# Performance work log

Hardware: AMD Instinct MI355X
Metric: run time of the kernel (lower is better)

## Reference

```python
import jax, jax.numpy as jnp
import numpy as np

N_NODES = 50000
N_EDGES = 800000
IN_DIM = 256
OUT_DIM = 128


def setup_inputs() -> dict:
    key = jax.random.key(0)
    k1, k2, k3, k4, k5 = jax.random.split(key, 5)
    adj_rows = jax.random.randint(k1, (N_EDGES,), 0, N_NODES, dtype=jnp.int32)
    adj_cols = jax.random.randint(k2, (N_EDGES,), 0, N_NODES, dtype=jnp.int32)
    adj_vals = jax.random.uniform(k3, (N_EDGES,), dtype=jnp.float32)
    x = jax.random.normal(k4, (N_NODES, IN_DIM), dtype=jnp.float32)
    # kaiming_normal-ish init for weight
    W = jax.random.normal(k5, (IN_DIM, OUT_DIM), dtype=jnp.float32) * np.sqrt(2.0 / IN_DIM)
    b = jnp.zeros((OUT_DIM,), dtype=jnp.float32)
    return {"adj_rows": adj_rows, "adj_cols": adj_cols, "adj_vals": adj_vals,
            "x": x, "W": W, "b": b}


def reference(adj_rows, adj_cols, adj_vals, x, W, b):
    # support = X @ W  (dense GEMM)
    support = x @ W  # [N, OUT_DIM]
    # sparse A @ support via edge-parallel gather + segment-sum (COO SpMM)
    msgs = adj_vals[:, None] * support[adj_cols]  # [E, OUT_DIM]
    out = jax.ops.segment_sum(msgs, adj_rows, num_segments=x.shape[0])
    return out + b
```

## Files before the change

kernel.cpp:

```cpp
#include <hip/hip_runtime.h>
#include <hip/hip_bf16.h>

#define N_NODES 50000
#define N_EDGES 800000
#define IN_DIM  256
#define OUT_DIM 128

#define NBINS        256
#define ROWS_PER_BIN 196
#define BIN_CAP      3600
#define EPB          2048
#define NB_BIN       391
#define NB_GEMM      1563
#define APITCH       264

typedef __bf16 bf16x8 __attribute__((ext_vector_type(8)));
typedef float  f32x4  __attribute__((ext_vector_type(4)));

__device__ __forceinline__ unsigned bin_of(unsigned r) { return (r * 85599u) >> 24; }
__device__ __forceinline__ float blo(unsigned u) { return __uint_as_float(u << 16); }
__device__ __forceinline__ float bhi(unsigned u) { return __uint_as_float(u & 0xffff0000u); }

#define WT_OFF   0
#define SUP_OFF  65536
#define BIN_OFF  12865536
#define CUR_OFF  20238336

__global__ void k_prep(const float* __restrict__ W, __bf16* __restrict__ Wt,
                       int* __restrict__ bin_cursor) {
    int t = blockIdx.x * 256 + threadIdx.x;
    if (t < 32768) { int n = t >> 8, k = t & 255; Wt[t] = (__bf16)W[k * OUT_DIM + n]; }
    if (t < NBINS) bin_cursor[t] = t * BIN_CAP;
}

__global__ __launch_bounds__(256) void k_fused(const float* __restrict__ x,
                                               const __bf16* __restrict__ Wt,
                                               unsigned* __restrict__ sup32,
                                               const int* __restrict__ rows,
                                               const int* __restrict__ cols,
                                               const float* __restrict__ vals,
                                               int* __restrict__ bin_cursor,
                                               int2* __restrict__ binbuf) {
    __shared__ union {
        struct {
            int2 stage[EPB];
            int  cnt[NBINS], off[NBINS], base[NBINS], cur[NBINS], s[NBINS];
        } bin;
        __bf16 a[32 * APITCH];
    } sh;
    int t = threadIdx.x;

    if (blockIdx.x < NB_BIN) {
        long e0 = (long)blockIdx.x * EPB;
        sh.bin.cnt[t] = 0;
        __syncthreads();

#pragma unroll
        for (int k = 0; k < EPB / 256; ++k) {
            long e = e0 + k * 256 + t;
            if (e < N_EDGES) atomicAdd(&sh.bin.cnt[bin_of((unsigned)rows[e])], 1);
        }
        __syncthreads();

        int v = sh.bin.cnt[t];
        sh.bin.s[t] = v; __syncthreads();
#pragma unroll
        for (int o = 1; o < 256; o <<= 1) {
            int xv = (t >= o) ? sh.bin.s[t - o] : 0;
            __syncthreads();
            sh.bin.s[t] += xv;
            __syncthreads();
        }
        sh.bin.off[t] = sh.bin.s[t] - v;
        sh.bin.cur[t] = sh.bin.s[t] - v;
        sh.bin.base[t] = atomicAdd(&bin_cursor[t], v);
        __syncthreads();

#pragma unroll
        for (int k = 0; k < EPB / 256; ++k) {
            long e = e0 + k * 256 + t;
            if (e < N_EDGES) {
                unsigned r = (unsigned)rows[e];
                unsigned c = (unsigned)cols[e];
                float    w = vals[e];
                int pos = atomicAdd(&sh.bin.cur[bin_of(r)], 1);
                sh.bin.stage[pos] = make_int2((int)((r << 16) | c), __float_as_int(w));
            }
        }
        __syncthreads();

        long rem = N_EDGES - e0;
        int nblk = rem < EPB ? (int)rem : EPB;
        for (int i = t; i < nblk; i += 256) {
            int2 rec = sh.bin.stage[i];
            unsigned bn = bin_of(((unsigned)rec.x) >> 16);
            int dst = sh.bin.base[bn] + (i - sh.bin.off[bn]);
            if (dst < (int)(bn + 1) * BIN_CAP)
                binbuf[dst] = rec;
        }
    } else {
        int  gb = blockIdx.x - NB_BIN;
        int  tp = gb * 2;
        long r0 = (long)tp * 16;

        const float4* xv = (const float4*)(x + r0 * IN_DIM);
#pragma unroll
        for (int it = 0; it < 8; ++it) {
            int idx = it * 256 + t;
            int row = idx >> 6;
            int col = idx & 63;
            if (r0 + row < N_NODES) {
                float4 f = xv[idx];
                __bf16 c0 = (__bf16)f.x, c1 = (__bf16)f.y;
                __bf16 c2 = (__bf16)f.z, c3 = (__bf16)f.w;
                unsigned lo = (unsigned)*(unsigned short*)&c0 |
                              ((unsigned)*(unsigned short*)&c1 << 16);
                unsigned hi = (unsigned)*(unsigned short*)&c2 |
                              ((unsigned)*(unsigned short*)&c3 << 16);
                *(uint2*)(&sh.a[row * APITCH + col * 4]) = make_uint2(lo, hi);
            }
        }
        __syncthreads();

        int wave = t >> 6;
        int lane = t & 63;
        int tile = tp + (wave >> 1);
        if (tile >= 3125) return;
        int h    = wave & 1;
        int a    = h * 2;
        int m    = lane & 15;
        int quad = lane >> 4;

        f32x4 acc0 = (f32x4){0,0,0,0}, acc1 = (f32x4){0,0,0,0};
        f32x4 acc2 = (f32x4){0,0,0,0}, acc3 = (f32x4){0,0,0,0};

        const __bf16* ap  = sh.a + ((wave >> 1) * 16 + m) * APITCH + quad * 8;
        const __bf16* wp  = Wt + m * IN_DIM + quad * 8;
        const __bf16* wp0 = wp + (a)     * 16 * IN_DIM;
        const __bf16* wp1 = wp + (a + 1) * 16 * IN_DIM;
        const __bf16* wp2 = wp + (a + 4) * 16 * IN_DIM;
        const __bf16* wp3 = wp + (a + 5) * 16 * IN_DIM;

#pragma unroll
        for (int ks = 0; ks < 8; ++ks) {
            bf16x8 af = *(const bf16x8*)(ap + ks * 32);
            bf16x8 b0 = *(const bf16x8*)(wp0 + ks * 32);
            bf16x8 b1 = *(const bf16x8*)(wp1 + ks * 32);
            bf16x8 b2 = *(const bf16x8*)(wp2 + ks * 32);
            bf16x8 b3 = *(const bf16x8*)(wp3 + ks * 32);
            acc0 = __builtin_amdgcn_mfma_f32_16x16x32_bf16(af, b0, acc0, 0, 0, 0);
            acc1 = __builtin_amdgcn_mfma_f32_16x16x32_bf16(af, b1, acc1, 0, 0, 0);
            acc2 = __builtin_amdgcn_mfma_f32_16x16x32_bf16(af, b2, acc2, 0, 0, 0);
            acc3 = __builtin_amdgcn_mfma_f32_16x16x32_bf16(af, b3, acc3, 0, 0, 0);
        }

        unsigned* op = sup32 + (long)tile * 16 * 64;
#pragma unroll
        for (int r = 0; r < 4; ++r) {
            __bf16 l0 = (__bf16)acc0[r], h0 = (__bf16)acc2[r];
            __bf16 l1 = (__bf16)acc1[r], h1 = (__bf16)acc3[r];
            unsigned w0 = (unsigned)*(unsigned short*)&l0 |
                          ((unsigned)*(unsigned short*)&h0 << 16);
            unsigned w1 = (unsigned)*(unsigned short*)&l1 |
                          ((unsigned)*(unsigned short*)&h1 << 16);
            op[(quad * 4 + r) * 64 + (a)     * 16 + m] = w0;
            op[(quad * 4 + r) * 64 + (a + 1) * 16 + m] = w1;
        }
    }
}

__global__ __launch_bounds__(1024) void k_sg(const int* __restrict__ bin_cursor,
                                             const int2* __restrict__ binbuf,
                                             const unsigned* __restrict__ sup,
                                             const float* __restrict__ bias,
                                             float* __restrict__ out) {
    __shared__ int2 stage[BIN_CAP];
    __shared__ int2 sorted_[BIN_CAP];
    __shared__ int  cnt[256], off[256], cur[256], s[256];
    int b = blockIdx.x, t = threadIdx.x;
    int row0 = b * ROWS_PER_BIN;

    int n = bin_cursor[b] - b * BIN_CAP;
    n = n < 0 ? 0 : (n > BIN_CAP ? BIN_CAP : n);
    const int2* seg = binbuf + (long)b * BIN_CAP;

    if (t < 256) cnt[t] = 0;
    __syncthreads();

    for (int i = t; i < n; i += 1024) {
        int2 rec = seg[i];
        stage[i] = rec;
        atomicAdd(&cnt[(int)(((unsigned)rec.x) >> 16) - row0], 1);
    }
    __syncthreads();

    int v = 0;
    if (t < 256) { v = cnt[t]; s[t] = v; }
    __syncthreads();
#pragma unroll
    for (int o = 1; o < 256; o <<= 1) {
        int xv = 0;
        if (t < 256 && t >= o) xv = s[t - o];
        __syncthreads();
        if (t < 256) s[t] += xv;
        __syncthreads();
    }
    if (t < 256) { off[t] = s[t] - v; cur[t] = 0; }
    __syncthreads();

    for (int i = t; i < n; i += 1024) {
        int2 rec = stage[i];
        int rl = (int)(((unsigned)rec.x) >> 16) - row0;
        sorted_[off[rl] + atomicAdd(&cur[rl], 1)] = rec;
    }
    __syncthreads();

    int wave = t >> 6, lane = t & 63;
    float bb0 = bias[lane], bb1 = bias[64 + lane];

    for (int rl = wave; rl < ROWS_PER_BIN; rl += 16) {
        int row = row0 + rl;
        if (row >= N_NODES) continue;
        int st = off[rl], nd = cnt[rl];
        float a0 = 0.f, a1 = 0.f;
        int i = 0;
        for (; i + 8 <= nd; i += 8) {
            int2 e[8]; unsigned u[8];
#pragma unroll
            for (int j = 0; j < 8; ++j) e[j] = sorted_[st + i + j];
#pragma unroll
            for (int j = 0; j < 8; ++j)
                u[j] = sup[(long)(((unsigned)e[j].x) & 0xffffu) * 64 + lane];
#pragma unroll
            for (int j = 0; j < 8; ++j) {
                float vv = __int_as_float(e[j].y);
                a0 += vv * blo(u[j]); a1 += vv * bhi(u[j]);
            }
        }
        for (; i < nd; ++i) {
            int2 ev = sorted_[st + i];
            unsigned uu = sup[(long)(((unsigned)ev.x) & 0xffffu) * 64 + lane];
            float vv = __int_as_float(ev.y);
            a0 += vv * blo(uu); a1 += vv * bhi(uu);
        }
        out[(long)row * 128 + lane]      = a0 + bb0;
        out[(long)row * 128 + 64 + lane] = a1 + bb1;
    }
}

extern "C" void kernel_launch(void* const* d_in, const int* in_sizes, int n_in,
                              void* d_out, int out_size, void* d_ws, size_t ws_size,
                              hipStream_t stream) {
    const int*   adj_rows = (const int*)  d_in[0];
    const int*   adj_cols = (const int*)  d_in[1];
    const float* adj_vals = (const float*)d_in[2];
    const float* x        = (const float*)d_in[3];
    const float* W        = (const float*)d_in[4];
    const float* b        = (const float*)d_in[5];
    float* out = (float*)d_out;

    char* ws = (char*)d_ws;
    __bf16*   Wt         = (__bf16*)  (ws + WT_OFF);
    unsigned* sup32      = (unsigned*)(ws + SUP_OFF);
    int2*     binbuf     = (int2*)    (ws + BIN_OFF);
    int*      bin_cursor = (int*)     (ws + CUR_OFF);

    k_prep <<<128, 256, 0, stream>>>(W, Wt, bin_cursor);
    k_fused<<<NB_BIN + NB_GEMM, 256, 0, stream>>>(x, Wt, sup32,
                                                  adj_rows, adj_cols, adj_vals,
                                                  bin_cursor, binbuf);
    k_sg   <<<NBINS, 1024, 0, stream>>>(bin_cursor, binbuf, sup32, b, out);
}
```

Baseline: 171.9 us.

## Fuse all stages into one persistent cooperative kernel with grid syncs

Replaces the three launches with a single cooperative persistent kernel of 256 blocks of 1024 threads. The blocks loop over binning and GEMM jobs, grid-sync, then do the per-bin sort and gather. Bins are halved in size (512 bins of 98 rows) and GEMM jobs now cover 64 rows per block. The aim is to remove launch gaps and tail idle time between stages. The cost is that persistent blocks may underutilize the GPU: there are only 512 sort jobs for 256 blocks, and large 1024-thread blocks cap occupancy. If the cooperative launch fails, it falls back to three separate launches.

```diff
diff --git a/kernel.cpp b/kernel.cpp
--- a/kernel.cpp
+++ b/kernel.cpp
@@ -1,250 +1,305 @@
 #include <hip/hip_runtime.h>
 #include <hip/hip_bf16.h>
+#include <hip/hip_cooperative_groups.h>
+
+namespace cg = cooperative_groups;
 
 #define N_NODES 50000
 #define N_EDGES 800000
 #define IN_DIM  256
 #define OUT_DIM 128
 
-#define NBINS        256
-#define ROWS_PER_BIN 196
-#define BIN_CAP      3600
-#define EPB          2048
-#define NB_BIN       391
-#define NB_GEMM      1563
-#define APITCH       264
+#define NBINS    512
+#define RPB      98
+#define BIN_CAP  1900
+#define EPB      2048
+#define NBJOBS   391
+#define NGJOBS   782
+#define NJOBS    (NBJOBS + NGJOBS)
+#define APITCH   264
 
 typedef __bf16 bf16x8 __attribute__((ext_vector_type(8)));
 typedef float  f32x4  __attribute__((ext_vector_type(4)));
 
-__device__ __forceinline__ unsigned bin_of(unsigned r) { return (r * 85599u) >> 24; }
+__device__ __forceinline__ unsigned bin_of(unsigned r) {
+    return (unsigned)(((unsigned long long)r * 171197ull) >> 24);
+}
 __device__ __forceinline__ float blo(unsigned u) { return __uint_as_float(u << 16); }
 __device__ __forceinline__ float bhi(unsigned u) { return __uint_as_float(u & 0xffff0000u); }
 
 #define WT_OFF   0
 #define SUP_OFF  65536
 #define BIN_OFF  12865536
-#define CUR_OFF  20238336
-
-__global__ void k_prep(const float* __restrict__ W, __bf16* __restrict__ Wt,
-                       int* __restrict__ bin_cursor) {
-    int t = blockIdx.x * 256 + threadIdx.x;
-    if (t < 32768) { int n = t >> 8, k = t & 255; Wt[t] = (__bf16)W[k * OUT_DIM + n]; }
-    if (t < NBINS) bin_cursor[t] = t * BIN_CAP;
-}
-
-__global__ __launch_bounds__(256) void k_fused(const float* __restrict__ x,
-                                               const __bf16* __restrict__ Wt,
-                                               unsigned* __restrict__ sup32,
-                                               const int* __restrict__ rows,
-                                               const int* __restrict__ cols,
-                                               const float* __restrict__ vals,
-                                               int* __restrict__ bin_cursor,
-                                               int2* __restrict__ binbuf) {
-    __shared__ union {
-        struct {
-            int2 stage[EPB];
-            int  cnt[NBINS], off[NBINS], base[NBINS], cur[NBINS], s[NBINS];
-        } bin;
-        __bf16 a[32 * APITCH];
-    } sh;
-    int t = threadIdx.x;
-
-    if (blockIdx.x < NB_BIN) {
-        long e0 = (long)blockIdx.x * EPB;
-        sh.bin.cnt[t] = 0;
-        __syncthreads();
-
-#pragma unroll
-        for (int k = 0; k < EPB / 256; ++k) {
-            long e = e0 + k * 256 + t;
-            if (e < N_EDGES) atomicAdd(&sh.bin.cnt[bin_of((unsigned)rows[e])], 1);
-        }
-        __syncthreads();
-
-        int v = sh.bin.cnt[t];
-        sh.bin.s[t] = v; __syncthreads();
-#pragma unroll
-        for (int o = 1; o < 256; o <<= 1) {
-            int xv = (t >= o) ? sh.bin.s[t - o] : 0;
-            __syncthreads();
-            sh.bin.s[t] += xv;
-            __syncthreads();
-        }
-        sh.bin.off[t] = sh.bin.s[t] - v;
-        sh.bin.cur[t] = sh.bin.s[t] - v;
+#define CUR_OFF  20647936
+
+struct ShBin {
+    int2 stage[EPB];
+    int  cnt[NBINS], off[NBINS], base[NBINS], cur[NBINS], s[NBINS];
+};
+struct ShSrt {
+    int2 stage[BIN_CAP];
+    int2 sorted_[BIN_CAP];
+    int  cnt[128], off[128], cur[128], s[128];
+};
+union Sh {
+    __bf16 a[64 * APITCH];
+    ShBin  bin;
+    ShSrt  srt;
+};
+
+__device__ __forceinline__ void do_prep(int g, const float* __restrict__ W,
+                                        __bf16* __restrict__ Wt,
+                                        int* __restrict__ bin_cursor) {
+    if (g < 32768) { int n = g >> 8, k = g & 255; Wt[g] = (__bf16)W[k * OUT_DIM + n]; }
+    if (g < NBINS) bin_cursor[g] = g * BIN_CAP;
+}
+
+__device__ __forceinline__ void do_bin_job(Sh& sh, int t, int jb,
+                                           const int* __restrict__ rows,
+                                           const int* __restrict__ cols,
+                                           const float* __restrict__ vals,
+                                           int* __restrict__ bin_cursor,
+                                           int2* __restrict__ binbuf) {
+    long e0 = (long)jb * EPB;
+    if (t < NBINS) sh.bin.cnt[t] = 0;
+    __syncthreads();
+#pragma unroll
+    for (int k = 0; k < 2; ++k) {
+        long e = e0 + k * 1024 + t;
+        if (e < N_EDGES) atomicAdd(&sh.bin.cnt[bin_of((unsigned)rows[e])], 1);
+    }
+    __syncthreads();
+    int v = 0;
+    if (t < NBINS) { v = sh.bin.cnt[t]; sh.bin.s[t] = v; }
+    __syncthreads();
+#pragma unroll
+    for (int o = 1; o < NBINS; o <<= 1) {
+        int xv = 0;
+        if (t < NBINS && t >= o) xv = sh.bin.s[t - o];
+        __syncthreads();
+        if (t < NBINS) sh.bin.s[t] += xv;
+        __syncthreads();
+    }
+    if (t < NBINS) {
+        sh.bin.off[t]  = sh.bin.s[t] - v;
+        sh.bin.cur[t]  = sh.bin.s[t] - v;
         sh.bin.base[t] = atomicAdd(&bin_cursor[t], v);
-        __syncthreads();
-
-#pragma unroll
-        for (int k = 0; k < EPB / 256; ++k) {
-            long e = e0 + k * 256 + t;
-            if (e < N_EDGES) {
-                unsigned r = (unsigned)rows[e];
-                unsigned c = (unsigned)cols[e];
-                float    w = vals[e];
-                int pos = atomicAdd(&sh.bin.cur[bin_of(r)], 1);
-                sh.bin.stage[pos] = make_int2((int)((r << 16) | c), __float_as_int(w));
-            }
-        }
-        __syncthreads();
-
-        long rem = N_EDGES - e0;
-        int nblk = rem < EPB ? (int)rem : EPB;
-        for (int i = t; i < nblk; i += 256) {
-            int2 rec = sh.bin.stage[i];
-            unsigned bn = bin_of(((unsigned)rec.x) >> 16);
-            int dst = sh.bin.base[bn] + (i - sh.bin.off[bn]);
-            if (dst < (int)(bn + 1) * BIN_CAP)
-                binbuf[dst] = rec;
-        }
-    } else {
-        int  gb = blockIdx.x - NB_BIN;
-        int  tp = gb * 2;
-        long r0 = (long)tp * 16;
-
-        const float4* xv = (const float4*)(x + r0 * IN_DIM);
-#pragma unroll
-        for (int it = 0; it < 8; ++it) {
-            int idx = it * 256 + t;
-            int row = idx >> 6;
-            int col = idx & 63;
-            if (r0 + row < N_NODES) {
-                float4 f = xv[idx];
-                __bf16 c0 = (__bf16)f.x, c1 = (__bf16)f.y;
-                __bf16 c2 = (__bf16)f.z, c3 = (__bf16)f.w;
-                unsigned lo = (unsigned)*(unsigned short*)&c0 |
-                              ((unsigned)*(unsigned short*)&c1 << 16);
-                unsigned hi = (unsigned)*(unsigned short*)&c2 |
-                              ((unsigned)*(unsigned short*)&c3 << 16);
-                *(uint2*)(&sh.a[row * APITCH + col * 4]) = make_uint2(lo, hi);
-            }
-        }
-        __syncthreads();
-
-        int wave = t >> 6;
-        int lane = t & 63;
-        int tile = tp + (wave >> 1);
-        if (tile >= 3125) return;
-        int h    = wave & 1;
-        int a    = h * 2;
-        int m    = lane & 15;
-        int quad = lane >> 4;
-
-        f32x4 acc0 = (f32x4){0,0,0,0}, acc1 = (f32x4){0,0,0,0};
-        f32x4 acc2 = (f32x4){0,0,0,0}, acc3 = (f32x4){0,0,0,0};
-
-        const __bf16* ap  = sh.a + ((wave >> 1) * 16 + m) * APITCH + quad * 8;
-        const __bf16* wp  = Wt + m * IN_DIM + quad * 8;
-        const __bf16* wp0 = wp + (a)     * 16 * IN_DIM;
-        const __bf16* wp1 = wp + (a + 1) * 16 * IN_DIM;
-        const __bf16* wp2 = wp + (a + 4) * 16 * IN_DIM;
-        const __bf16* wp3 = wp + (a + 5) * 16 * IN_DIM;
-
+    }
+    __syncthreads();
+#pragma unroll
+    for (int k = 0; k < 2; ++k) {
+        long e = e0 + k * 1024 + t;
+        if (e < N_EDGES) {
+            unsigned r = (unsigned)rows[e];
+            unsigned c = (unsigned)cols[e];
+            float    w = vals[e];
+            int pos = atomicAdd(&sh.bin.cur[bin_of(r)], 1);
+            sh.bin.stage[pos] = make_int2((int)((r << 16) | c), __float_as_int(w));
+        }
+    }
+    __syncthreads();
+    long rem = N_EDGES - e0;
+    int nblk = rem < EPB ? (int)rem : EPB;
+    for (int i = t; i < nblk; i += 1024) {
+        int2 rec = sh.bin.stage[i];
+        unsigned bn = bin_of(((unsigned)rec.x) >> 16);
+        int dst = sh.bin.base[bn] + (i - sh.bin.off[bn]);
+        if (dst < (int)(bn + 1) * BIN_CAP)
+            binbuf[dst] = rec;
+    }
+}
+
+__device__ __forceinline__ void do_gemm_job(Sh& sh, int t, int gs,
+                                            const float* __restrict__ x,
+                                            const __bf16* __restrict__ Wt,
+                                            unsigned* __restrict__ sup32) {
+    long r0 = (long)gs * 64;
+    const float4* xv = (const float4*)(x + r0 * IN_DIM);
+#pragma unroll
+    for (int it = 0; it < 4; ++it) {
+        int idx = it * 1024 + t;
+        int row = idx >> 6;
+        int col = idx & 63;
+        if (r0 + row < N_NODES) {
+            float4 f = xv[idx];
+            __bf16 c0 = (__bf16)f.x, c1 = (__bf16)f.y;
+            __bf16 c2 = (__bf16)f.z, c3 = (__bf16)f.w;
+            unsigned lo = (unsigned)*(unsigned short*)&c0 |
+                          ((unsigned)*(unsigned short*)&c1 << 16);
+            unsigned hi = (unsigned)*(unsigned short*)&c2 |
+                          ((unsigned)*(unsigned short*)&c3 << 16);
+            *(uint2*)(&sh.a[row * APITCH + col * 4]) = make_uint2(lo, hi);
+        }
+    }
+    __syncthreads();
+
+    int wave = t >> 6, lane = t & 63;
+    int tl   = wave >> 2;
+    int q    = wave & 3;
+    int tile = gs * 4 + tl;
+    if (tile < 3125) {
+        int m = lane & 15, quad = lane >> 4;
+        f32x4 accL = (f32x4){0,0,0,0}, accH = (f32x4){0,0,0,0};
+        const __bf16* ap  = sh.a + (tl * 16 + m) * APITCH + quad * 8;
+        const __bf16* wpL = Wt + (q)     * 16 * IN_DIM + m * IN_DIM + quad * 8;
+        const __bf16* wpH = Wt + (q + 4) * 16 * IN_DIM + m * IN_DIM + quad * 8;
 #pragma unroll
         for (int ks = 0; ks < 8; ++ks) {
-            bf16x8 af = *(const bf16x8*)(ap + ks * 32);
-            bf16x8 b0 = *(const bf16x8*)(wp0 + ks * 32);
-            bf16x8 b1 = *(const bf16x8*)(wp1 + ks * 32);
-            bf16x8 b2 = *(const bf16x8*)(wp2 + ks * 32);
-            bf16x8 b3 = *(const bf16x8*)(wp3 + ks * 32);
-            acc0 = __builtin_amdgcn_mfma_f32_16x16x32_bf16(af, b0, acc0, 0, 0, 0);
-            acc1 = __builtin_amdgcn_mfma_f32_16x16x32_bf16(af, b1, acc1, 0, 0, 0);
-            acc2 = __builtin_amdgcn_mfma_f32_16x16x32_bf16(af, b2, acc2, 0, 0, 0);
-            acc3 = __builtin_amdgcn_mfma_f32_16x16x32_bf16(af, b3, acc3, 0, 0, 0);
-        }
-
+            bf16x8 af = *(const bf16x8*)(ap  + ks * 32);
+            bf16x8 bL = *(const bf16x8*)(wpL + ks * 32);
+            bf16x8 bH = *(const bf16x8*)(wpH + ks * 32);
+            accL = __builtin_amdgcn_mfma_f32_16x16x32_bf16(af, bL, accL, 0, 0, 0);
+            accH = __builtin_amdgcn_mfma_f32_16x16x32_bf16(af, bH, accH, 0, 0, 0);
+        }
         unsigned* op = sup32 + (long)tile * 16 * 64;
 #pragma unroll
         for (int r = 0; r < 4; ++r) {
-            __bf16 l0 = (__bf16)acc0[r], h0 = (__bf16)acc2[r];
-            __bf16 l1 = (__bf16)acc1[r], h1 = (__bf16)acc3[r];
-            unsigned w0 = (unsigned)*(unsigned short*)&l0 |
-                          ((unsigned)*(unsigned short*)&h0 << 16);
-            unsigned w1 = (unsigned)*(unsigned short*)&l1 |
-                          ((unsigned)*(unsigned short*)&h1 << 16);
-            op[(quad * 4 + r) * 64 + (a)     * 16 + m] = w0;
-            op[(quad * 4 + r) * 64 + (a + 1) * 16 + m] = w1;
-        }
-    }
-}
-
-__global__ __launch_bounds__(1024) void k_sg(const int* __restrict__ bin_cursor,
-                                             const int2* __restrict__ binbuf,
-                                             const unsigned* __restrict__ sup,
-                                             const float* __restrict__ bias,
-                                             float* __restrict__ out) {
-    __shared__ int2 stage[BIN_CAP];
-    __shared__ int2 sorted_[BIN_CAP];
-    __shared__ int  cnt[256], off[256], cur[256], s[256];
-    int b = blockIdx.x, t = threadIdx.x;
-    int row0 = b * ROWS_PER_BIN;
-
+            __bf16 lo = (__bf16)accL[r], hi = (__bf16)accH[r];
+            unsigned w = (unsigned)*(unsigned short*)&lo |
+                         ((unsigned)*(unsigned short*)&hi << 16);
+            op[(quad * 4 + r) * 64 + q * 16 + m] = w;
+        }
+    }
+}
+
+__device__ __forceinline__ void do_srt(Sh& sh, int t, int b,
+                                       const int* __restrict__ bin_cursor,
+                                       const int2* __restrict__ binbuf,
+                                       const unsigned* __restrict__ sup32,
+                                       const float* __restrict__ bias,
+                                       float* __restrict__ out) {
+    int row0 = b * RPB;
     int n = bin_cursor[b] - b * BIN_CAP;
     n = n < 0 ? 0 : (n > BIN_CAP ? BIN_CAP : n);
     const int2* seg = binbuf + (long)b * BIN_CAP;
 
-    if (t < 256) cnt[t] = 0;
-    __syncthreads();
-
+    if (t < 128) sh.srt.cnt[t] = 0;
+    __syncthreads();
     for (int i = t; i < n; i += 1024) {
         int2 rec = seg[i];
-        stage[i] = rec;
-        atomicAdd(&cnt[(int)(((unsigned)rec.x) >> 16) - row0], 1);
-    }
-    __syncthreads();
-
+        sh.srt.stage[i] = rec;
+        atomicAdd(&sh.srt.cnt[(int)(((unsigned)rec.x) >> 16) - row0], 1);
+    }
+    __syncthreads();
     int v = 0;
-    if (t < 256) { v = cnt[t]; s[t] = v; }
-    __syncthreads();
-#pragma unroll
-    for (int o = 1; o < 256; o <<= 1) {
+    if (t < 128) { v = sh.srt.cnt[t]; sh.srt.s[t] = v; }
+    __syncthreads();
+#pragma unroll
+    for (int o = 1; o < 128; o <<= 1) {
         int xv = 0;
-        if (t < 256 && t >= o) xv = s[t - o];
-        __syncthreads();
-        if (t < 256) s[t] += xv;
-        __syncthreads();
-    }
-    if (t < 256) { off[t] = s[t] - v; cur[t] = 0; }
-    __syncthreads();
-
+        if (t < 128 && t >= o) xv = sh.srt.s[t - o];
+        __syncthreads();
+        if (t < 128) sh.srt.s[t] += xv;
+        __syncthreads();
+    }
+    if (t < 128) { sh.srt.off[t] = sh.srt.s[t] - v; sh.srt.cur[t] = 0; }
+    __syncthreads();
     for (int i = t; i < n; i += 1024) {
-        int2 rec = stage[i];
+        int2 rec = sh.srt.stage[i];
         int rl = (int)(((unsigned)rec.x) >> 16) - row0;
-        sorted_[off[rl] + atomicAdd(&cur[rl], 1)] = rec;
+        sh.srt.sorted_[sh.srt.off[rl] + atomicAdd(&sh.srt.cur[rl], 1)] = rec;
     }
     __syncthreads();
 
     int wave = t >> 6, lane = t & 63;
     float bb0 = bias[lane], bb1 = bias[64 + lane];
-
-    for (int rl = wave; rl < ROWS_PER_BIN; rl += 16) {
+    for (int rl = wave; rl < RPB; rl += 16) {
         int row = row0 + rl;
-        if (row >= N_NODES) continue;
-        int st = off[rl], nd = cnt[rl];
-        float a0 = 0.f, a1 = 0.f;
-        int i = 0;
-        for (; i + 8 <= nd; i += 8) {
-            int2 e[8]; unsigned u[8];
-#pragma unroll
-            for (int j = 0; j < 8; ++j) e[j] = sorted_[st + i + j];
-#pragma unroll
-            for (int j = 0; j < 8; ++j)
-                u[j] = sup[(long)(((unsigned)e[j].x) & 0xffffu) * 64 + lane];
-#pragma unroll
-            for (int j = 0; j < 8; ++j) {
-                float vv = __int_as_float(e[j].y);
-                a0 += vv * blo(u[j]); a1 += vv * bhi(u[j]);
+        if (row < N_NODES) {
+            int st = sh.srt.off[rl], nd = sh.srt.cnt[rl];
+            float a0 = 0.f, a1 = 0.f;
+            int i = 0;
+            for (; i + 8 <= nd; i += 8) {
+                int2 e[8]; unsigned u[8];
+#pragma unroll
+                for (int jj = 0; jj < 8; ++jj) e[jj] = sh.srt.sorted_[st + i + jj];
+#pragma unroll
+                for (int jj = 0; jj < 8; ++jj)
+                    u[jj] = sup32[(long)(((unsigned)e[jj].x) & 0xffffu) * 64 + lane];
+#pragma unroll
+                for (int jj = 0; jj < 8; ++jj) {
+                    float vv = __int_as_float(e[jj].y);
+                    a0 += vv * blo(u[jj]); a1 += vv * bhi(u[jj]);
+                }
             }
-        }
-        for (; i < nd; ++i) {
-            int2 ev = sorted_[st + i];
-            unsigned uu = sup[(long)(((unsigned)ev.x) & 0xffffu) * 64 + lane];
-            float vv = __int_as_float(ev.y);
-            a0 += vv * blo(uu); a1 += vv * bhi(uu);
-        }
-        out[(long)row * 128 + lane]      = a0 + bb0;
-        out[(long)row * 128 + 64 + lane] = a1 + bb1;
+            for (; i < nd; ++i) {
+                int2 ev = sh.srt.sorted_[st + i];
+                unsigned uu = sup32[(long)(((unsigned)ev.x) & 0xffffu) * 64 + lane];
+                float vv = __int_as_float(ev.y);
+                a0 += vv * blo(uu); a1 += vv * bhi(uu);
+            }
+            out[(long)row * 128 + lane]      = a0 + bb0;
+            out[(long)row * 128 + 64 + lane] = a1 + bb1;
+        }
+    }
+}
+
+__global__ __launch_bounds__(1024, 4) void k_all(const float* __restrict__ x,
+                                                 const float* __restrict__ W,
+                                                 __bf16* __restrict__ Wt,
+                                                 unsigned* __restrict__ sup32,
+                                                 const int* __restrict__ rows,
+                                                 const int* __restrict__ cols,
+                                                 const float* __restrict__ vals,
+                                                 int* __restrict__ bin_cursor,
+                                                 int2* __restrict__ binbuf,
+                                                 const float* __restrict__ bias,
+                                                 float* __restrict__ out) {
+    __shared__ Sh sh;
+    cg::grid_group grid = cg::this_grid();
+    int t = threadIdx.x;
+
+    do_prep(blockIdx.x * 1024 + t, W, Wt, bin_cursor);
+    __threadfence();
+    grid.sync();
+
+    for (int j = blockIdx.x; j < NJOBS; j += gridDim.x) {
+        __syncthreads();
+        if (j < NBJOBS) do_bin_job(sh, t, j, rows, cols, vals, bin_cursor, binbuf);
+        else            do_gemm_job(sh, t, j - NBJOBS, x, Wt, sup32);
+    }
+    __threadfence();
+    grid.sync();
+
+    for (int b = blockIdx.x; b < NBINS; b += gridDim.x) {
+        __syncthreads();
+        do_srt(sh, t, b, bin_cursor, binbuf, sup32, bias, out);
+    }
+}
+
+__global__ __launch_bounds__(1024) void k_p1(const float* __restrict__ W,
+                                             __bf16* __restrict__ Wt,
+                                             int* __restrict__ bin_cursor) {
+    do_prep(blockIdx.x * 1024 + threadIdx.x, W, Wt, bin_cursor);
+}
+
+__global__ __launch_bounds__(1024, 4) void k_p2(const float* __restrict__ x,
+                                                const __bf16* __restrict__ Wt,
+                                                unsigned* __restrict__ sup32,
+                                                const int* __restrict__ rows,
+                                                const int* __restrict__ cols,
+                                                const float* __restrict__ vals,
+                                                int* __restrict__ bin_cursor,
+                                                int2* __restrict__ binbuf) {
+    __shared__ Sh sh;
+    int t = threadIdx.x;
+    for (int j = blockIdx.x; j < NJOBS; j += gridDim.x) {
+        __syncthreads();
+        if (j < NBJOBS) do_bin_job(sh, t, j, rows, cols, vals, bin_cursor, binbuf);
+        else            do_gemm_job(sh, t, j - NBJOBS, x, Wt, sup32);
+    }
+}
+
+__global__ __launch_bounds__(1024, 4) void k_p3(const int* __restrict__ bin_cursor,
+                                                const int2* __restrict__ binbuf,
+                                                const unsigned* __restrict__ sup32,
+                                                const float* __restrict__ bias,
+                                                float* __restrict__ out) {
+    __shared__ Sh sh;
+    int t = threadIdx.x;
+    for (int b = blockIdx.x; b < NBINS; b += gridDim.x) {
+        __syncthreads();
+        do_srt(sh, t, b, bin_cursor, binbuf, sup32, bias, out);
     }
 }
 
@@ -265,9 +320,18 @@
     int2*     binbuf     = (int2*)    (ws + BIN_OFF);
     int*      bin_cursor = (int*)     (ws + CUR_OFF);
 
-    k_prep <<<128, 256, 0, stream>>>(W, Wt, bin_cursor);
-    k_fused<<<NB_BIN + NB_GEMM, 256, 0, stream>>>(x, Wt, sup32,
-                                                  adj_rows, adj_cols, adj_vals,
-                                                  bin_cursor, binbuf);
-    k_sg   <<<NBINS, 1024, 0, stream>>>(bin_cursor, binbuf, sup32, b, out);
-}
+    void* args[] = { (void*)&x, (void*)&W, (void*)&Wt, (void*)&sup32,
+                     (void*)&adj_rows, (void*)&adj_cols, (void*)&adj_vals,
+                     (void*)&bin_cursor, (void*)&binbuf, (void*)&b, (void*)&out };
+
+    hipError_t err = hipLaunchCooperativeKernel((const void*)k_all,
+                                                dim3(256), dim3(1024),
+                                                args, 0, stream);
+    if (err != hipSuccess) {
+        (void)hipGetLastError();
+        k_p1<<<32,  1024, 0, stream>>>(W, Wt, bin_cursor);
+        k_p2<<<256, 1024, 0, stream>>>(x, Wt, sup32, adj_rows, adj_cols, adj_vals,
+                                       bin_cursor, binbuf);
+        k_p3<<<256, 1024, 0, stream>>>(bin_cursor, binbuf, sup32, b, out);
+    }
+}
```

Measured after the change: 399.4 us. 2.32x slower.
